# Kernel tuning notes

Measured on AMD Instinct MI355X. Metric: run time of the kernel, lower is better.

Reference implementation:

```python
import jax, jax.numpy as jnp
import numpy as np

B, N, D, H = 4, 1024, 768, 12
DH = D // H
HIDDEN = 4 * D
EPS = 1e-6


def _layernorm(x, g, b):
    mu = jnp.mean(x, axis=-1, keepdims=True)
    var = jnp.mean(jnp.square(x - mu), axis=-1, keepdims=True)
    return (x - mu) * jax.lax.rsqrt(var + EPS) * g + b


def setup_inputs() -> dict:
    key = jax.random.key(0)
    ks = jax.random.split(key, 8)
    s = 0.02  # init scale for weights
    return {
        "x": jax.random.normal(ks[0], (B, N, D), jnp.float32),
        "adj_bias": jax.random.normal(ks[1], (N, N), jnp.float32) * 0.1,
        "ln1_g": jnp.ones((D,), jnp.float32),
        "ln1_b": jnp.zeros((D,), jnp.float32),
        "qkv_w": jax.random.normal(ks[2], (D, 3 * D), jnp.float32) * s,
        "qkv_b": jnp.zeros((3 * D,), jnp.float32),
        "proj_w": jax.random.normal(ks[3], (D, D), jnp.float32) * s,
        "proj_b": jnp.zeros((D,), jnp.float32),
        "ln2_g": jnp.ones((D,), jnp.float32),
        "ln2_b": jnp.zeros((D,), jnp.float32),
        "fc1_w": jax.random.normal(ks[4], (D, HIDDEN), jnp.float32) * s,
        "fc1_b": jnp.zeros((HIDDEN,), jnp.float32),
        "fc2_w": jax.random.normal(ks[5], (HIDDEN, D), jnp.float32) * s,
        "fc2_b": jnp.zeros((D,), jnp.float32),
    }


def reference(x, adj_bias, ln1_g, ln1_b, qkv_w, qkv_b, proj_w, proj_b,
              ln2_g, ln2_b, fc1_w, fc1_b, fc2_w, fc2_b):
    scale = DH ** -0.5
    # --- attention with additive adjacency bias ---
    h = _layernorm(x, ln1_g, ln1_b)
    qkv = (h @ qkv_w + qkv_b).reshape(B, N, 3, H, DH)
    q, k, v = (jnp.moveaxis(qkv, 2, 0)[i].transpose(0, 2, 1, 3) for i in range(3))  # [B,H,N,DH]
    scores = jnp.einsum('bhqd,bhkd->bhqk', q, k) * scale + adj_bias[None, None]
    w = jax.nn.softmax(scores, axis=-1)
    attn = jnp.einsum('bhqk,bhkd->bhqd', w, v)          # [B,H,N,DH]
    attn = attn.transpose(0, 2, 1, 3).reshape(B, N, D)  # [B,N,D]
    x = x + (attn @ proj_w + proj_b)
    # --- MLP ---
    h2 = _layernorm(x, ln2_g, ln2_b)
    m = jax.nn.gelu(h2 @ fc1_w + fc1_b, approximate=False) @ fc2_w + fc2_b
    return x + m
```

## Files before the change

### kernel.cpp

```cpp
#include <hip/hip_runtime.h>
#include <cstdint>
#include <cstring>

typedef unsigned short u16;
typedef __attribute__((ext_vector_type(8))) short short8;
typedef __attribute__((ext_vector_type(4))) float float4v;

#define BB 4
#define NN 1024
#define DD 768
#define HH 12
#define DHH 64
#define HID 3072
#define MM (BB*NN)

__device__ __forceinline__ u16 f2b(float f) {
  unsigned int u = __float_as_uint(f);
  u += 0x7FFF + ((u >> 16) & 1);
  return (u16)(u >> 16);
}
__device__ __forceinline__ float b2f(u16 h) {
  return __uint_as_float(((unsigned int)h) << 16);
}

__device__ __forceinline__ void gll16(const void* g, void* l) {
  __builtin_amdgcn_global_load_lds(
      (const __attribute__((address_space(1))) unsigned int*)g,
      (__attribute__((address_space(3))) unsigned int*)l, 16, 0, 0);
}

__global__ __launch_bounds__(256)
void prep_k(const float* __restrict__ qkvw, const float* __restrict__ projw,
            const float* __restrict__ fc1w, const float* __restrict__ fc2w,
            const float* __restrict__ adj,
            u16* __restrict__ wtqkv, u16* __restrict__ wtproj,
            u16* __restrict__ wtfc1, u16* __restrict__ wtfc2,
            u16* __restrict__ adjP) {
  __shared__ float tile[32][33];
  const int id = blockIdx.x, t = threadIdx.x;
  if (id < 6912) {
    const float* w; u16* wt; int K, N, tid;
    if (id < 1728)      { w = qkvw;  wt = wtqkv;  K = DD;  N = 3 * DD; tid = id; }
    else if (id < 2304) { w = projw; wt = wtproj; K = DD;  N = DD;     tid = id - 1728; }
    else if (id < 4608) { w = fc1w;  wt = wtfc1;  K = DD;  N = HID;    tid = id - 2304; }
    else                { w = fc2w;  wt = wtfc2;  K = HID; N = DD;     tid = id - 4608; }
    const int ntiles = N / 32;
    const int n0 = (tid % ntiles) * 32, k0 = (tid / ntiles) * 32;
    const int tx = t & 31, ty = t >> 5;
#pragma unroll
    for (int i = 0; i < 4; i++)
      tile[ty + i * 8][tx] = w[(size_t)(k0 + ty + i * 8) * N + n0 + tx];
    __syncthreads();
#pragma unroll
    for (int i = 0; i < 4; i++)
      wt[(size_t)(n0 + ty + i * 8) * K + k0 + tx] = f2b(tile[tx][ty + i * 8]);
  } else {
    const int aid = id - 6912;
    const int qt = aid >> 4, kt = aid & 15;
    const int wv = t >> 6, q4 = (t >> 4) & 3, m15 = t & 15;
    u16 v[16];
#pragma unroll
    for (int ct = 0; ct < 4; ct++)
#pragma unroll
      for (int r = 0; r < 4; r++)
        v[ct * 4 + r] =
            f2b(adj[(size_t)(qt * 64 + wv * 16 + q4 * 4 + r) * NN + kt * 64 + ct * 16 + m15]);
    u16* dst = adjP + (size_t)aid * 4096 + t * 16;
    *(uint4*)dst = *(const uint4*)&v[0];
    *(uint4*)(dst + 8) = *(const uint4*)&v[8];
  }
}

__global__ __launch_bounds__(256)
void ln_k(const float* __restrict__ x, const float* __restrict__ g,
          const float* __restrict__ b, u16* __restrict__ o) {
  const int row = blockIdx.x, t = threadIdx.x;
  const float* xr = x + (size_t)row * DD;
  float v0 = xr[t], v1 = xr[t + 256], v2 = xr[t + 512];
  float s = v0 + v1 + v2;
  float s2 = v0 * v0 + v1 * v1 + v2 * v2;
#pragma unroll
  for (int off = 32; off > 0; off >>= 1) {
    s += __shfl_down(s, off);
    s2 += __shfl_down(s2, off);
  }
  __shared__ float rs[4], rs2[4], bc[2];
  const int lane = t & 63, wv = t >> 6;
  if (lane == 0) { rs[wv] = s; rs2[wv] = s2; }
  __syncthreads();
  if (t == 0) {
    float ts = rs[0] + rs[1] + rs[2] + rs[3];
    float ts2 = rs2[0] + rs2[1] + rs2[2] + rs2[3];
    float mean = ts * (1.f / DD);
    float var = ts2 * (1.f / DD) - mean * mean;
    bc[0] = mean;
    bc[1] = rsqrtf(var + 1e-6f);
  }
  __syncthreads();
  const float mean = bc[0], rstd = bc[1];
  u16* orow = o + (size_t)row * DD;
  orow[t]       = f2b((v0 - mean) * rstd * g[t]       + b[t]);
  orow[t + 256] = f2b((v1 - mean) * rstd * g[t + 256] + b[t + 256]);
  orow[t + 512] = f2b((v2 - mean) * rstd * g[t + 512] + b[t + 512]);
}

template <int MODE, int TN, int BK, int NC>
__global__ __launch_bounds__(256, (TN == 128 && BK == 64) ? 2 : 4)
void gemm_k(const u16* __restrict__ A, const u16* __restrict__ Bt,
            const float* __restrict__ bias, const float* __restrict__ resid,
            float* __restrict__ outf, u16* __restrict__ outb,
            u16* __restrict__ outq, u16* __restrict__ outk, u16* __restrict__ outv,
            int K) {
  __shared__ u16 As[2][128 * BK];
  __shared__ u16 Bs[2][TN * BK];
  constexpr int JM = TN / 32;
  constexpr int KK = BK / 32;
  constexpr int SLOTS = BK / 8;
  constexpr int AI = BK / 4;
  constexpr int BI = TN * BK / 512;
  constexpr int VC = (AI + BI) / 4;
  constexpr int NB = NC / TN;
  constexpr int RN = NB / 2;

  const int id = blockIdx.x;
  const int xcd = id & 7, idx = id >> 3;
  const int tileN = ((xcd & 1) * RN + idx % RN) * TN;
  const int tileM = ((xcd >> 1) * 8 + idx / RN) * 128;

  const int lane = threadIdx.x & 63, wave = threadIdx.x >> 6;
  const int wrow = (wave >> 1) * 64, wcol = (wave & 1) * (TN / 2);
  const int m15 = lane & 15, q4 = lane >> 4;
  const int rkey = (BK == 32) ? ((m15 >> 1) & 3) : (m15 & 7);

  float4v acc[4][JM];
#pragma unroll
  for (int i = 0; i < 4; i++)
#pragma unroll
    for (int j = 0; j < JM; j++) acc[i][j] = (float4v)0.f;

  auto stage = [&](int kt, int buf) {
    const int kk0 = kt * BK;
#pragma unroll
    for (int q = wave; q < AI; q += 4) {
      const int c = q * 64 + lane;
      const int row = c / SLOTS, slot = c % SLOTS;
      const int key = (BK == 32) ? ((row >> 1) & 3) : (row & 7);
      gll16(A + (size_t)(tileM + row) * K + kk0 + (slot ^ key) * 8, &As[buf][q * 512]);
    }
#pragma unroll
    for (int q = wave; q < BI; q += 4) {
      const int c = q * 64 + lane;
      const int row = c / SLOTS, slot = c % SLOTS;
      const int key = (BK == 32) ? ((row >> 1) & 3) : (row & 7);
      gll16(Bt + (size_t)(tileN + row) * K + kk0 + (slot ^ key) * 8, &Bs[buf][q * 512]);
    }
  };

  const int T = K / BK;
  stage(0, 0);
  for (int kt = 0; kt < T; ++kt) {
    const int cur = kt & 1;
    if (kt + 1 < T) {
      stage(kt + 1, cur ^ 1);
      asm volatile("s_waitcnt vmcnt(%0)\n\ts_barrier" :: "n"(VC) : "memory");
    } else {
      asm volatile("s_waitcnt vmcnt(0)\n\ts_barrier" ::: "memory");
    }
    short8 af[4][KK], bfr[JM][KK];
#pragma unroll
    for (int i = 0; i < 4; i++)
#pragma unroll
      for (int kk = 0; kk < KK; kk++)
        af[i][kk] = *(const short8*)(
            &As[cur][(wrow + i * 16 + m15) * BK + (((kk * 4 + q4) ^ rkey)) * 8]);
#pragma unroll
    for (int j = 0; j < JM; j++)
#pragma unroll
      for (int kk = 0; kk < KK; kk++)
        bfr[j][kk] = *(const short8*)(
            &Bs[cur][(wcol + j * 16 + m15) * BK + (((kk * 4 + q4) ^ rkey)) * 8]);
#pragma unroll
    for (int i = 0; i < 4; i++)
#pragma unroll
      for (int j = 0; j < JM; j++)
#pragma unroll
        for (int kk = 0; kk < KK; kk++)
          acc[i][j] =
              __builtin_amdgcn_mfma_f32_16x16x32_bf16(af[i][kk], bfr[j][kk], acc[i][j], 0, 0, 0);
    asm volatile("s_waitcnt lgkmcnt(0)\n\ts_barrier" ::: "memory");
  }

#pragma unroll
  for (int i = 0; i < 4; i++) {
#pragma unroll
    for (int j = 0; j < JM; j++) {
      const int col = tileN + wcol + j * 16 + m15;
#pragma unroll
      for (int r = 0; r < 4; r++) {
        const int row = tileM + wrow + i * 16 + q4 * 4 + r;
        float v = acc[i][j][r] + bias[col];
        if (MODE == 1) {
          outf[(size_t)row * NC + col] = resid[(size_t)row * NC + col] + v;
        } else if (MODE == 2) {
          float gv = 0.5f * v * (1.f + erff(v * 0.70710678f));
          outb[(size_t)row * NC + col] = f2b(gv);
        } else {
          const int three = col / DD, hh = (col % DD) >> 6, dh = col & 63;
          const int bb = row >> 10, nn = row & 1023;
          if (three == 2) {
            outv[(((size_t)(bb * HH + hh)) * DHH + dh) * NN + nn] = f2b(v);
          } else {
            const size_t idx2 = (((size_t)(bb * HH + hh)) * NN + nn) * DHH + dh;
            (three == 0 ? outq : outk)[idx2] = f2b(v);
          }
        }
      }
    }
  }
}

__global__ __launch_bounds__(256, 4)
void attn_k(const u16* __restrict__ qw, const u16* __restrict__ kw,
            const u16* __restrict__ vtw, const u16* __restrict__ adjP,
            u16* __restrict__ out) {
  __shared__ u16 Ks[64][72];
  __shared__ u16 Vt[64][72];
  __shared__ u16 Pb[4][16][72];

  const int id = blockIdx.x;
  const int bh = (id & 7) * 6 + ((id >> 3) >> 4);
  const int qt = (id >> 3) & 15;
  const int t = threadIdx.x, lane = t & 63, wave = t >> 6;
  const int m15 = lane & 15, q4 = lane >> 4;

  const u16* qrow = qw + ((size_t)bh * NN + qt * 64 + wave * 16 + m15) * DHH;
  const short8 qf0 = *(const short8*)(qrow + q4 * 8);
  const short8 qf1 = *(const short8*)(qrow + 32 + q4 * 8);

  float lreg[4] = {0.f, 0.f, 0.f, 0.f};
  float4v o[4];
#pragma unroll
  for (int ct = 0; ct < 4; ct++) o[ct] = (float4v)0.f;

  const u16* kbase0 = kw + (size_t)bh * NN * DHH;
  const u16* vtbase0 = vtw + (size_t)bh * DHH * NN;
  const u16* abase = adjP + (size_t)qt * 16 * 4096 + t * 16;

  const int r0 = t >> 3;
  const int c80 = (t & 7) * 8;

  uint4 kr0 = *(const uint4*)(kbase0 + r0 * 64 + c80);
  uint4 kr1 = *(const uint4*)(kbase0 + (r0 + 32) * 64 + c80);
  uint4 vr0 = *(const uint4*)(vtbase0 + (size_t)r0 * NN + c80);
  uint4 vr1 = *(const uint4*)(vtbase0 + (size_t)(r0 + 32) * NN + c80);

  for (int kt = 0; kt < 16; kt++) {
    __syncthreads();
    *(uint4*)&Ks[r0][c80] = kr0;
    *(uint4*)&Ks[r0 + 32][c80] = kr1;
    *(uint4*)&Vt[r0][c80] = vr0;
    *(uint4*)&Vt[r0 + 32][c80] = vr1;
    __syncthreads();
    if (kt < 15) {
      const u16* kb = kbase0 + (size_t)(kt + 1) * 64 * DHH;
      const u16* vb = vtbase0 + (kt + 1) * 64;
      kr0 = *(const uint4*)(kb + r0 * 64 + c80);
      kr1 = *(const uint4*)(kb + (r0 + 32) * 64 + c80);
      vr0 = *(const uint4*)(vb + (size_t)r0 * NN + c80);
      vr1 = *(const uint4*)(vb + (size_t)(r0 + 32) * NN + c80);
    }
    u16 av[16];
    const u16* ap = abase + (size_t)kt * 4096;
    *(uint4*)&av[0] = *(const uint4*)ap;
    *(uint4*)&av[8] = *(const uint4*)(ap + 8);

    float4v s[4];
#pragma unroll
    for (int ct = 0; ct < 4; ct++) s[ct] = (float4v)0.f;
#pragma unroll
    for (int ct = 0; ct < 4; ct++) {
      short8 b = *(const short8*)&Ks[ct * 16 + m15][q4 * 8];
      s[ct] = __builtin_amdgcn_mfma_f32_16x16x32_bf16(qf0, b, s[ct], 0, 0, 0);
    }
#pragma unroll
    for (int ct = 0; ct < 4; ct++) {
      short8 b = *(const short8*)&Ks[ct * 16 + m15][32 + q4 * 8];
      s[ct] = __builtin_amdgcn_mfma_f32_16x16x32_bf16(qf1, b, s[ct], 0, 0, 0);
    }

#pragma unroll
    for (int ct = 0; ct < 4; ct++)
#pragma unroll
      for (int r = 0; r < 4; r++) {
        float v = s[ct][r] * 0.125f + b2f(av[ct * 4 + r]);
        u16 pb = f2b(__expf(v));
        Pb[wave][q4 * 4 + r][ct * 16 + m15] = pb;
        lreg[r] += b2f(pb);
      }

    asm volatile("s_waitcnt lgkmcnt(0)" ::: "memory");

    short8 a0 = *(const short8*)&Pb[wave][m15][q4 * 8];
    short8 a1 = *(const short8*)&Pb[wave][m15][32 + q4 * 8];
#pragma unroll
    for (int ct = 0; ct < 4; ct++) {
      short8 b = *(const short8*)&Vt[ct * 16 + m15][q4 * 8];
      o[ct] = __builtin_amdgcn_mfma_f32_16x16x32_bf16(a0, b, o[ct], 0, 0, 0);
    }
#pragma unroll
    for (int ct = 0; ct < 4; ct++) {
      short8 b = *(const short8*)&Vt[ct * 16 + m15][32 + q4 * 8];
      o[ct] = __builtin_amdgcn_mfma_f32_16x16x32_bf16(a1, b, o[ct], 0, 0, 0);
    }
  }

#pragma unroll
  for (int off = 1; off < 16; off <<= 1)
#pragma unroll
    for (int r = 0; r < 4; r++) lreg[r] += __shfl_xor(lreg[r], off);

  const int bb2 = bh / HH, hh = bh % HH;
  const int row0 = qt * 64 + wave * 16 + q4 * 4;
#pragma unroll
  for (int ct = 0; ct < 4; ct++)
#pragma unroll
    for (int r = 0; r < 4; r++)
      out[((size_t)(bb2 * NN + row0 + r)) * DD + hh * 64 + ct * 16 + m15] =
          f2b(o[ct][r] / lreg[r]);
}

extern "C" void kernel_launch(void* const* d_in, const int* in_sizes, int n_in,
                              void* d_out, int out_size, void* d_ws, size_t ws_size,
                              hipStream_t stream) {
  const float* x     = (const float*)d_in[0];
  const float* adj   = (const float*)d_in[1];
  const float* ln1g  = (const float*)d_in[2];
  const float* ln1b  = (const float*)d_in[3];
  const float* qkvw  = (const float*)d_in[4];
  const float* qkvb  = (const float*)d_in[5];
  const float* projw = (const float*)d_in[6];
  const float* projb = (const float*)d_in[7];
  const float* ln2g  = (const float*)d_in[8];
  const float* ln2b  = (const float*)d_in[9];
  const float* fc1w  = (const float*)d_in[10];
  const float* fc1b  = (const float*)d_in[11];
  const float* fc2w  = (const float*)d_in[12];
  const float* fc2b  = (const float*)d_in[13];
  float* out = (float*)d_out;

  char* ws = (char*)d_ws;
  u16* wtqkv = (u16*)ws;  ws += (size_t)DD * (3 * DD) * 2;
  u16* wtproj = (u16*)ws; ws += (size_t)DD * DD * 2;
  u16* wtfc1 = (u16*)ws;  ws += (size_t)DD * HID * 2;
  u16* wtfc2 = (u16*)ws;  ws += (size_t)HID * DD * 2;
  u16* adjP = (u16*)ws;   ws += (size_t)NN * NN * 2;
  u16* hbuf = (u16*)ws;   ws += (size_t)MM * DD * 2;
  u16* qws = (u16*)ws;    ws += (size_t)MM * DD * 2;
  u16* kws = (u16*)ws;    ws += (size_t)MM * DD * 2;
  u16* vtws = (u16*)ws;   ws += (size_t)MM * DD * 2;
  u16* attnb = (u16*)ws;  ws += (size_t)MM * DD * 2;
  u16* h2buf = (u16*)ws;  ws += (size_t)MM * DD * 2;
  u16* a1buf = (u16*)ws;  ws += (size_t)MM * HID * 2;

  prep_k<<<7168, 256, 0, stream>>>(qkvw, projw, fc1w, fc2w, adj,
                                   wtqkv, wtproj, wtfc1, wtfc2, adjP);

  ln_k<<<MM, 256, 0, stream>>>(x, ln1g, ln1b, hbuf);

  gemm_k<0, 128, 64, 3 * DD><<<((3 * DD) / 128) * (MM / 128), 256, 0, stream>>>(
      hbuf, wtqkv, qkvb, nullptr, nullptr, nullptr, qws, kws, vtws, DD);

  attn_k<<<(NN / 64) * (BB * HH), 256, 0, stream>>>(qws, kws, vtws, adjP, attnb);

  gemm_k<1, 64, 64, DD><<<(DD / 64) * (MM / 128), 256, 0, stream>>>(
      attnb, wtproj, projb, x, out, nullptr, nullptr, nullptr, nullptr, DD);

  ln_k<<<MM, 256, 0, stream>>>(out, ln2g, ln2b, h2buf);

  gemm_k<2, 128, 64, HID><<<(HID / 128) * (MM / 128), 256, 0, stream>>>(
      h2buf, wtfc1, fc1b, nullptr, nullptr, a1buf, nullptr, nullptr, nullptr, DD);

  gemm_k<1, 64, 64, DD><<<(DD / 64) * (MM / 128), 256, 0, stream>>>(
      a1buf, wtfc2, fc2b, out, out, nullptr, nullptr, nullptr, nullptr, HID);
}
```

Measured before the change: 294.3 us.

## Shrink GEMM tiles to 64-row, 2-wave blocks and fuse LN1 into prep kernel

The GEMM kernel moves from 128-row tiles on 4 waves to 64-row tiles on 2 waves (128 threads), and the QKV and FC1 GEMMs also drop BK from 64 to 32. This doubles the block count so the machine fills better and each block holds less LDS. The first LayerNorm is merged into the weight-prep kernel as extra blocks, which removes one launch and lets it run alongside the weight conversion. The cost is less data reuse per block, more global loads per FLOP, and more K-loop barrier iterations.

```diff
diff --git a/kernel.cpp b/kernel.cpp
--- a/kernel.cpp
+++ b/kernel.cpp
@@ -30,13 +30,15 @@
 }
 
 __global__ __launch_bounds__(256)
-void prep_k(const float* __restrict__ qkvw, const float* __restrict__ projw,
-            const float* __restrict__ fc1w, const float* __restrict__ fc2w,
-            const float* __restrict__ adj,
-            u16* __restrict__ wtqkv, u16* __restrict__ wtproj,
-            u16* __restrict__ wtfc1, u16* __restrict__ wtfc2,
-            u16* __restrict__ adjP) {
+void front_k(const float* __restrict__ qkvw, const float* __restrict__ projw,
+             const float* __restrict__ fc1w, const float* __restrict__ fc2w,
+             const float* __restrict__ adj, const float* __restrict__ x,
+             const float* __restrict__ ln1g, const float* __restrict__ ln1b,
+             u16* __restrict__ wtqkv, u16* __restrict__ wtproj,
+             u16* __restrict__ wtfc1, u16* __restrict__ wtfc2,
+             u16* __restrict__ adjP, u16* __restrict__ hbuf) {
   __shared__ float tile[32][33];
+  __shared__ float rs[4], rs2[4], bc[2];
   const int id = blockIdx.x, t = threadIdx.x;
   if (id < 6912) {
     const float* w; u16* wt; int K, N, tid;
@@ -54,7 +56,7 @@
 #pragma unroll
     for (int i = 0; i < 4; i++)
       wt[(size_t)(n0 + ty + i * 8) * K + k0 + tx] = f2b(tile[tx][ty + i * 8]);
-  } else {
+  } else if (id < 7168) {
     const int aid = id - 6912;
     const int qt = aid >> 4, kt = aid & 15;
     const int wv = t >> 6, q4 = (t >> 4) & 3, m15 = t & 15;
@@ -68,6 +70,34 @@
     u16* dst = adjP + (size_t)aid * 4096 + t * 16;
     *(uint4*)dst = *(const uint4*)&v[0];
     *(uint4*)(dst + 8) = *(const uint4*)&v[8];
+  } else {
+    const int row = id - 7168;
+    const float* xr = x + (size_t)row * DD;
+    float v0 = xr[t], v1 = xr[t + 256], v2 = xr[t + 512];
+    float s = v0 + v1 + v2;
+    float s2 = v0 * v0 + v1 * v1 + v2 * v2;
+#pragma unroll
+    for (int off = 32; off > 0; off >>= 1) {
+      s += __shfl_down(s, off);
+      s2 += __shfl_down(s2, off);
+    }
+    const int lane = t & 63, wv = t >> 6;
+    if (lane == 0) { rs[wv] = s; rs2[wv] = s2; }
+    __syncthreads();
+    if (t == 0) {
+      float ts = rs[0] + rs[1] + rs[2] + rs[3];
+      float ts2 = rs2[0] + rs2[1] + rs2[2] + rs2[3];
+      float mean = ts * (1.f / DD);
+      float var = ts2 * (1.f / DD) - mean * mean;
+      bc[0] = mean;
+      bc[1] = rsqrtf(var + 1e-6f);
+    }
+    __syncthreads();
+    const float mean = bc[0], rstd = bc[1];
+    u16* orow = hbuf + (size_t)row * DD;
+    orow[t]       = f2b((v0 - mean) * rstd * ln1g[t]       + ln1b[t]);
+    orow[t + 256] = f2b((v1 - mean) * rstd * ln1g[t + 256] + ln1b[t + 256]);
+    orow[t + 512] = f2b((v2 - mean) * rstd * ln1g[t + 512] + ln1b[t + 512]);
   }
 }
 
@@ -105,30 +135,32 @@
 }
 
 template <int MODE, int TN, int BK, int NC>
-__global__ __launch_bounds__(256, (TN == 128 && BK == 64) ? 2 : 4)
+__global__ __launch_bounds__(128, 2)
 void gemm_k(const u16* __restrict__ A, const u16* __restrict__ Bt,
             const float* __restrict__ bias, const float* __restrict__ resid,
             float* __restrict__ outf, u16* __restrict__ outb,
             u16* __restrict__ outq, u16* __restrict__ outk, u16* __restrict__ outv,
             int K) {
-  __shared__ u16 As[2][128 * BK];
+  constexpr int BM = 64;
+  __shared__ u16 As[2][BM * BK];
   __shared__ u16 Bs[2][TN * BK];
   constexpr int JM = TN / 32;
   constexpr int KK = BK / 32;
   constexpr int SLOTS = BK / 8;
-  constexpr int AI = BK / 4;
-  constexpr int BI = TN * BK / 512;
-  constexpr int VC = (AI + BI) / 4;
+  constexpr int AI = BM * SLOTS / 64;
+  constexpr int BI = TN * SLOTS / 64;
+  constexpr int VC = (AI + BI) / 2;
   constexpr int NB = NC / TN;
   constexpr int RN = NB / 2;
+  constexpr int MB = MM / BM;
 
   const int id = blockIdx.x;
   const int xcd = id & 7, idx = id >> 3;
   const int tileN = ((xcd & 1) * RN + idx % RN) * TN;
-  const int tileM = ((xcd >> 1) * 8 + idx / RN) * 128;
+  const int tileM = ((xcd >> 1) * (MB / 4) + idx / RN) * BM;
 
   const int lane = threadIdx.x & 63, wave = threadIdx.x >> 6;
-  const int wrow = (wave >> 1) * 64, wcol = (wave & 1) * (TN / 2);
+  const int wcol = wave * (TN / 2);
   const int m15 = lane & 15, q4 = lane >> 4;
   const int rkey = (BK == 32) ? ((m15 >> 1) & 3) : (m15 & 7);
 
@@ -141,14 +173,14 @@
   auto stage = [&](int kt, int buf) {
     const int kk0 = kt * BK;
 #pragma unroll
-    for (int q = wave; q < AI; q += 4) {
+    for (int q = wave; q < AI; q += 2) {
       const int c = q * 64 + lane;
       const int row = c / SLOTS, slot = c % SLOTS;
       const int key = (BK == 32) ? ((row >> 1) & 3) : (row & 7);
       gll16(A + (size_t)(tileM + row) * K + kk0 + (slot ^ key) * 8, &As[buf][q * 512]);
     }
 #pragma unroll
-    for (int q = wave; q < BI; q += 4) {
+    for (int q = wave; q < BI; q += 2) {
       const int c = q * 64 + lane;
       const int row = c / SLOTS, slot = c % SLOTS;
       const int key = (BK == 32) ? ((row >> 1) & 3) : (row & 7);
@@ -172,7 +204,7 @@
 #pragma unroll
       for (int kk = 0; kk < KK; kk++)
         af[i][kk] = *(const short8*)(
-            &As[cur][(wrow + i * 16 + m15) * BK + (((kk * 4 + q4) ^ rkey)) * 8]);
+            &As[cur][(i * 16 + m15) * BK + (((kk * 4 + q4) ^ rkey)) * 8]);
 #pragma unroll
     for (int j = 0; j < JM; j++)
 #pragma unroll
@@ -197,7 +229,7 @@
       const int col = tileN + wcol + j * 16 + m15;
 #pragma unroll
       for (int r = 0; r < 4; r++) {
-        const int row = tileM + wrow + i * 16 + q4 * 4 + r;
+        const int row = tileM + i * 16 + q4 * 4 + r;
         float v = acc[i][j][r] + bias[col];
         if (MODE == 1) {
           outf[(size_t)row * NC + col] = resid[(size_t)row * NC + col] + v;
@@ -362,24 +394,22 @@
   u16* h2buf = (u16*)ws;  ws += (size_t)MM * DD * 2;
   u16* a1buf = (u16*)ws;  ws += (size_t)MM * HID * 2;
 
-  prep_k<<<7168, 256, 0, stream>>>(qkvw, projw, fc1w, fc2w, adj,
-                                   wtqkv, wtproj, wtfc1, wtfc2, adjP);
-
-  ln_k<<<MM, 256, 0, stream>>>(x, ln1g, ln1b, hbuf);
-
-  gemm_k<0, 128, 64, 3 * DD><<<((3 * DD) / 128) * (MM / 128), 256, 0, stream>>>(
+  front_k<<<7168 + MM, 256, 0, stream>>>(qkvw, projw, fc1w, fc2w, adj, x, ln1g, ln1b,
+                                         wtqkv, wtproj, wtfc1, wtfc2, adjP, hbuf);
+
+  gemm_k<0, 128, 32, 3 * DD><<<((3 * DD) / 128) * (MM / 64), 128, 0, stream>>>(
       hbuf, wtqkv, qkvb, nullptr, nullptr, nullptr, qws, kws, vtws, DD);
 
   attn_k<<<(NN / 64) * (BB * HH), 256, 0, stream>>>(qws, kws, vtws, adjP, attnb);
 
-  gemm_k<1, 64, 64, DD><<<(DD / 64) * (MM / 128), 256, 0, stream>>>(
+  gemm_k<1, 64, 64, DD><<<(DD / 64) * (MM / 64), 128, 0, stream>>>(
       attnb, wtproj, projb, x, out, nullptr, nullptr, nullptr, nullptr, DD);
 
   ln_k<<<MM, 256, 0, stream>>>(out, ln2g, ln2b, h2buf);
 
-  gemm_k<2, 128, 64, HID><<<(HID / 128) * (MM / 128), 256, 0, stream>>>(
+  gemm_k<2, 128, 32, HID><<<(HID / 128) * (MM / 64), 128, 0, stream>>>(
       h2buf, wtfc1, fc1b, nullptr, nullptr, a1buf, nullptr, nullptr, nullptr, DD);
 
-  gemm_k<1, 64, 64, DD><<<(DD / 64) * (MM / 128), 256, 0, stream>>>(
+  gemm_k<1, 64, 64, DD><<<(DD / 64) * (MM / 64), 128, 0, stream>>>(
       a1buf, wtfc2, fc2b, out, out, nullptr, nullptr, nullptr, nullptr, HID);
 }
```

New measurement: 274.1 us. 1.07x faster.
